# Kernel tuning notes

Hardware: AMD Instinct MI355X
Metric: run time of the kernel (lower is better)

The kernel has to match this reference:

```python
import jax, jax.numpy as jnp
import numpy as np
import math

B, T, D, H = 2, 2048, 1024, 16
DK = D // H
NEG = -1e9  # finite stand-in for -inf causal fill inside the ALiBi bias


def make_alibi_bias(n_heads: int, seq_len: int) -> jnp.ndarray:
    # standard ALiBi slopes: 2^(-8*h/H) for h = 1..H
    slopes = 2.0 ** (-8.0 * (np.arange(1, n_heads + 1) / n_heads))  # [H]
    pos = np.arange(seq_len)
    dist = pos[None, :] - pos[:, None]  # [T,T], j - i
    bias = slopes[:, None, None] * dist[None, :, :]  # [H,T,T], <=0 below diag
    bias = np.where(dist[None] > 0, NEG, bias)  # causal: mask future
    return jnp.asarray(bias, dtype=jnp.float32)


def setup_inputs() -> dict:
    key = jax.random.key(0)
    ks = jax.random.split(key, 8)
    s = 0.02
    return {
        "query": jax.random.normal(ks[0], (B, T, D), jnp.float32),
        "key": jax.random.normal(ks[1], (B, T, D), jnp.float32),
        "value": jax.random.normal(ks[2], (B, T, D), jnp.float32),
        "alibi_bias": make_alibi_bias(H, T),
        "wq": jax.random.normal(ks[3], (D, D), jnp.float32) * s,
        "wk": jax.random.normal(ks[4], (D, D), jnp.float32) * s,
        "wv": jax.random.normal(ks[5], (D, D), jnp.float32) * s,
        "wo": jax.random.normal(ks[6], (D, D), jnp.float32) * s,
        "bo": jnp.zeros((D,), jnp.float32),
    }


def reference(query, key, value, alibi_bias, wq, wk, wv, wo, bo):
    b, tq, d = query.shape
    # linear projections (torch Linear: x @ W^T), split heads -> [B,H,T,d_k]
    def split(x, w):
        y = jnp.einsum('btd,ed->bte', x, w)
        return y.reshape(b, -1, H, DK).transpose(0, 2, 1, 3)
    Q, K, V = split(query, wq), split(key, wk), split(value, wv)
    # scores + ALiBi bias (bias already encodes causality)
    scores = jnp.einsum('bhqd,bhkd->bhqk', Q, K) / math.sqrt(DK)
    scores = scores + alibi_bias[None]  # broadcast over batch
    attn = jax.nn.softmax(scores, axis=-1)
    out = jnp.einsum('bhqk,bhkd->bhqd', attn, V)  # [B,H,Tq,d_k]
    out = out.transpose(0, 2, 1, 3).reshape(b, tq, d)
    return jnp.einsum('btd,ed->bte', out, wo) + bo
```

## Files before the change

kernel.cpp:

```cpp
#include <hip/hip_runtime.h>
#include <hip/hip_bf16.h>
#include <stdint.h>

#define Bc   2
#define Tc   2048
#define Dc   1024
#define Hc   16
#define DKc  64
#define BTc  4096
#define LOG2E 1.44269504088896f

typedef unsigned short u16;
typedef unsigned int u32;
typedef __attribute__((ext_vector_type(8))) short bf16x8;
typedef __attribute__((ext_vector_type(4))) float f32x4;
typedef __attribute__((ext_vector_type(2))) u32 u32x2;

static __device__ __forceinline__ u16 f2bf(float f) {
  union { float f; unsigned u; } v; v.f = f;
  unsigned r = v.u + 0x7fffu + ((v.u >> 16) & 1u);
  return (u16)(r >> 16);
}

static __device__ __forceinline__ u32 cvt_pk_bf16(float lo, float hi) {
  u32 r;
  asm volatile("v_cvt_pk_bf16_f32 %0, %1, %2" : "=v"(r) : "v"(lo), "v"(hi));
  return r;
}

static __device__ __forceinline__ f32x4 mfma16(bf16x8 a, bf16x8 b, f32x4 c) {
  return __builtin_amdgcn_mfma_f32_16x16x32_bf16(a, b, c, 0, 0, 0);
}

__global__ void conv_kernel(const float* __restrict__ q, const float* __restrict__ k,
                            const float* __restrict__ v, const float* __restrict__ wq,
                            const float* __restrict__ wk, const float* __restrict__ wv,
                            const float* __restrict__ wo,
                            u16* __restrict__ Xq, u16* __restrict__ Xk, u16* __restrict__ Xv,
                            u16* __restrict__ Wq, u16* __restrict__ Wk, u16* __restrict__ Wv,
                            u16* __restrict__ Wo) {
  int z = blockIdx.z, bx = blockIdx.x;
  const float* src; u16* dst; int i;
  if (bx < 4096) {
    if (z == 3) return;
    src = z == 0 ? q : z == 1 ? k : v;
    dst = z == 0 ? Xq : z == 1 ? Xk : Xv;
    i = bx * 256 + threadIdx.x;
  } else {
    src = z == 0 ? wq : z == 1 ? wk : z == 2 ? wv : wo;
    dst = z == 0 ? Wq : z == 1 ? Wk : z == 2 ? Wv : Wo;
    i = (bx - 4096) * 256 + threadIdx.x;
  }
  float4 f = ((const float4*)src)[i];
  ushort4 r; r.x = f2bf(f.x); r.y = f2bf(f.y); r.z = f2bf(f.z); r.w = f2bf(f.w);
  ((ushort4*)dst)[i] = r;
}

#define AS1 const __attribute__((address_space(1))) void*
#define AS3 __attribute__((address_space(3))) void*

__global__ __launch_bounds__(256) void gemm_proj(const u16* __restrict__ Xq, const u16* __restrict__ Xk,
                                                 const u16* __restrict__ Xv, const u16* __restrict__ Wq,
                                                 const u16* __restrict__ Wk, const u16* __restrict__ Wv,
                                                 u16* __restrict__ Qh, u16* __restrict__ Kh,
                                                 u16* __restrict__ VTo) {
  __shared__ u16 As[128 * 32];
  __shared__ u16 Bs[128 * 32];
  int z = blockIdx.z;
  const u16* A = z == 0 ? Xq : z == 1 ? Xk : Xv;
  const u16* W = z == 0 ? Wq : z == 1 ? Wk : Wv;
  u16* outp    = z == 0 ? Qh : z == 1 ? Kh : VTo;
  float scale = (z == 0) ? 0.125f * LOG2E : 1.0f;
  int tid = threadIdx.x;
  int lane = tid & 63, wave = tid >> 6;
  int ln = lane & 15, g = lane >> 4;
  int m0 = blockIdx.x * 128, n0 = blockIdx.y * 128;
  int wm = (wave >> 1) * 64, wn = (wave & 1) * 64;
  f32x4 acc[4][4] = {};
  int c0 = tid, c1 = tid + 256;
  const u16* gA0 = A + (size_t)(m0 + (c0 >> 2)) * 1024 + (c0 & 3) * 8;
  const u16* gA1 = A + (size_t)(m0 + (c1 >> 2)) * 1024 + (c1 & 3) * 8;
  const u16* gW0 = W + (size_t)(n0 + (c0 >> 2)) * 1024 + (c0 & 3) * 8;
  const u16* gW1 = W + (size_t)(n0 + (c1 >> 2)) * 1024 + (c1 & 3) * 8;
  for (int k0 = 0; k0 < 1024; k0 += 32) {
    __builtin_amdgcn_global_load_lds((AS1)(gA0 + k0), (AS3)(As + c0 * 8), 16, 0, 0);
    __builtin_amdgcn_global_load_lds((AS1)(gA1 + k0), (AS3)(As + c1 * 8), 16, 0, 0);
    __builtin_amdgcn_global_load_lds((AS1)(gW0 + k0), (AS3)(Bs + c0 * 8), 16, 0, 0);
    __builtin_amdgcn_global_load_lds((AS1)(gW1 + k0), (AS3)(Bs + c1 * 8), 16, 0, 0);
    __syncthreads();
    bf16x8 af[4], bfr[4];
#pragma unroll
    for (int mi = 0; mi < 4; ++mi) af[mi]  = *(const bf16x8*)&As[(wm + mi * 16 + ln) * 32 + g * 8];
#pragma unroll
    for (int ni = 0; ni < 4; ++ni) bfr[ni] = *(const bf16x8*)&Bs[(wn + ni * 16 + ln) * 32 + g * 8];
#pragma unroll
    for (int mi = 0; mi < 4; ++mi)
#pragma unroll
      for (int ni = 0; ni < 4; ++ni)
        acc[mi][ni] = mfma16(af[mi], bfr[ni], acc[mi][ni]);
    __syncthreads();
  }
  if (z == 2) {
#pragma unroll
    for (int mi = 0; mi < 4; ++mi)
#pragma unroll
      for (int ni = 0; ni < 4; ++ni) {
        int t0 = m0 + wm + mi * 16 + g * 4;
        int gn = n0 + wn + ni * 16 + ln;
        size_t bhead = ((size_t)(t0 >> 11)) * Hc + (gn >> 6);
        ushort4 pk;
        pk.x = f2bf(acc[mi][ni][0]); pk.y = f2bf(acc[mi][ni][1]);
        pk.z = f2bf(acc[mi][ni][2]); pk.w = f2bf(acc[mi][ni][3]);
        *(ushort4*)&outp[(bhead * DKc + (gn & 63)) * Tc + (t0 & 2047)] = pk;
      }
  } else {
#pragma unroll
    for (int mi = 0; mi < 4; ++mi)
#pragma unroll
      for (int ni = 0; ni < 4; ++ni)
#pragma unroll
        for (int r = 0; r < 4; ++r) {
          int gm = m0 + wm + mi * 16 + g * 4 + r;
          int gn = n0 + wn + ni * 16 + ln;
          size_t bhead = ((size_t)(gm >> 11)) * Hc + (gn >> 6);
          outp[(bhead * Tc + (gm & 2047)) * DKc + (gn & 63)] = f2bf(acc[mi][ni][r] * scale);
        }
  }
}

__global__ __launch_bounds__(256) void gemm_out(const u16* __restrict__ Ain, const u16* __restrict__ W,
                                                float* __restrict__ of, const float* __restrict__ bias) {
  __shared__ u16 As[64 * 32];
  __shared__ u16 Bs[128 * 32];
  int tid = threadIdx.x;
  int lane = tid & 63, wave = tid >> 6;
  int ln = lane & 15, g = lane >> 4;
  int m0 = blockIdx.x * 64, n0 = blockIdx.y * 128;
  int wm = (wave >> 1) * 32, wn = (wave & 1) * 64;
  f32x4 acc[2][4] = {};
  int ca = tid, cb0 = tid, cb1 = tid + 256;
  const u16* gA  = Ain + (size_t)(m0 + (ca  >> 2)) * 1024 + (ca  & 3) * 8;
  const u16* gW0 = W   + (size_t)(n0 + (cb0 >> 2)) * 1024 + (cb0 & 3) * 8;
  const u16* gW1 = W   + (size_t)(n0 + (cb1 >> 2)) * 1024 + (cb1 & 3) * 8;
  for (int k0 = 0; k0 < 1024; k0 += 32) {
    __builtin_amdgcn_global_load_lds((AS1)(gA  + k0), (AS3)(As + ca  * 8), 16, 0, 0);
    __builtin_amdgcn_global_load_lds((AS1)(gW0 + k0), (AS3)(Bs + cb0 * 8), 16, 0, 0);
    __builtin_amdgcn_global_load_lds((AS1)(gW1 + k0), (AS3)(Bs + cb1 * 8), 16, 0, 0);
    __syncthreads();
    bf16x8 af[2], bfr[4];
#pragma unroll
    for (int mi = 0; mi < 2; ++mi) af[mi]  = *(const bf16x8*)&As[(wm + mi * 16 + ln) * 32 + g * 8];
#pragma unroll
    for (int ni = 0; ni < 4; ++ni) bfr[ni] = *(const bf16x8*)&Bs[(wn + ni * 16 + ln) * 32 + g * 8];
#pragma unroll
    for (int mi = 0; mi < 2; ++mi)
#pragma unroll
      for (int ni = 0; ni < 4; ++ni)
        acc[mi][ni] = mfma16(af[mi], bfr[ni], acc[mi][ni]);
    __syncthreads();
  }
#pragma unroll
  for (int mi = 0; mi < 2; ++mi)
#pragma unroll
    for (int ni = 0; ni < 4; ++ni)
#pragma unroll
      for (int r = 0; r < 4; ++r) {
        int gm = m0 + wm + mi * 16 + g * 4 + r;
        int gn = n0 + wn + ni * 16 + ln;
        of[(size_t)gm * 1024 + gn] = acc[mi][ni][r] + bias[gn];
      }
}

__global__ __launch_bounds__(256, 2) void flash_attn(const u16* __restrict__ Qh,
                                                     const u16* __restrict__ Kh,
                                                     const u16* __restrict__ VT,
                                                     u16* __restrict__ O) {
  __shared__ u16 Ks[2][64 * 64];
  __shared__ u16 Vs[2][64 * 64];
  __shared__ u16 P_lds[8][16][64];
  int pid = blockIdx.x, bh = blockIdx.y;
  int qhi = 16 + pid, qlo = 15 - pid;
  int b = bh >> 4, h = bh & (Hc - 1);
  int tid = threadIdx.x, wave = tid >> 6, lane = tid & 63;
  int ln = lane & 15, g = lane >> 4;
  float slope2 = exp2f(-0.5f * (float)(h + 1)) * LOG2E;

  const u16* gK = Kh + (size_t)bh * Tc * DKc;
  const u16* gV = VT + (size_t)bh * DKc * Tc;
  int c0 = tid, c1 = tid + 256;
  int r0 = c0 >> 3, r1 = c1 >> 3;
  int e0 = ((c0 & 7) << 3) ^ ((r0 & 7) << 3);
  int e1 = ((c1 & 7) << 3) ^ ((r1 & 7) << 3);
  size_t kO0 = (size_t)r0 * DKc + e0, kO1 = (size_t)r1 * DKc + e1;
  size_t vO0 = (size_t)r0 * Tc + e0, vO1 = (size_t)r1 * Tc + e1;

#define STAGE(bufi, ks_) do {                                                                  \
    __builtin_amdgcn_global_load_lds((AS1)(gK + (size_t)(ks_) * DKc + kO0),                    \
                                     (AS3)(&Ks[bufi][c0 * 8]), 16, 0, 0);                      \
    __builtin_amdgcn_global_load_lds((AS1)(gK + (size_t)(ks_) * DKc + kO1),                    \
                                     (AS3)(&Ks[bufi][c1 * 8]), 16, 0, 0);                      \
    __builtin_amdgcn_global_load_lds((AS1)(gV + (size_t)(ks_) + vO0),                          \
                                     (AS3)(&Vs[bufi][c0 * 8]), 16, 0, 0);                      \
    __builtin_amdgcn_global_load_lds((AS1)(gV + (size_t)(ks_) + vO1),                          \
                                     (AS3)(&Vs[bufi][c1 * 8]), 16, 0, 0);                      \
  } while (0)

  int qlocal = wave * 16 + ln;
  int qgH = qhi * 64 + qlocal, qgL = qlo * 64 + qlocal;
  const u16* QpH = Qh + ((size_t)bh * Tc + qgH) * DKc;
  const u16* QpL = Qh + ((size_t)bh * Tc + qgL) * DKc;
  bf16x8 qfH0 = *(const bf16x8*)&QpH[g * 8];
  bf16x8 qfH1 = *(const bf16x8*)&QpH[32 + g * 8];
  bf16x8 qfL0 = *(const bf16x8*)&QpL[g * 8];
  bf16x8 qfL1 = *(const bf16x8*)&QpL[32 + g * 8];

  float vb[4][4];
#pragma unroll
  for (int j = 0; j < 4; ++j)
#pragma unroll
    for (int r = 0; r < 4; ++r)
      vb[j][r] = slope2 * (float)(j * 16 + g * 4 + r);

  f32x4 accH[4] = {}, accL[4] = {};
  float MH = -1e30f, LH = 0.f, ML = -1e30f, LL = 0.f;

  auto tile_step = [&](int buf, int ks, bool diag, bf16x8 qf0, bf16x8 qf1,
                       int qg, float& Mx, float& Lx, f32x4* accO, int pslot) {
    f32x4 s[4] = {};
    __builtin_amdgcn_s_setprio(1);
#pragma unroll
    for (int j = 0; j < 4; ++j) {
      int row = j * 16 + ln, sw = (row & 7) << 3;
      bf16x8 kf0 = *(const bf16x8*)&Ks[buf][row * DKc + ((g * 8) ^ sw)];
      bf16x8 kf1 = *(const bf16x8*)&Ks[buf][row * DKc + ((32 + g * 8) ^ sw)];
      s[j] = mfma16(kf0, qf0, s[j]);
      s[j] = mfma16(kf1, qf1, s[j]);
    }
    __builtin_amdgcn_s_setprio(0);
    float vv[4][4];
    float mloc = -1e30f;
#pragma unroll
    for (int j = 0; j < 4; ++j)
#pragma unroll
      for (int r = 0; r < 4; ++r) {
        float t = s[j][r] + vb[j][r];
        if (diag) t = (j * 16 + g * 4 + r > qlocal) ? -1e30f : t;
        vv[j][r] = t;
        mloc = fmaxf(mloc, t);
      }
    mloc = fmaxf(mloc, __shfl_xor(mloc, 16, 64));
    mloc = fmaxf(mloc, __shfl_xor(mloc, 32, 64));
    float cterm = slope2 * (float)(ks - qg);
    float mc = mloc + cterm;
    if (__any(mc > Mx)) {
      float newM = fmaxf(Mx, mc);
      float sc = __builtin_amdgcn_exp2f(Mx - newM);
      Mx = newM;
      Lx *= sc;
      float scb[4];
#pragma unroll
      for (int r = 0; r < 4; ++r) scb[r] = __shfl(sc, g * 4 + r, 64);
#pragma unroll
      for (int nd = 0; nd < 4; ++nd)
#pragma unroll
        for (int r = 0; r < 4; ++r) accO[nd][r] *= scb[r];
    }
    float dsub = Mx - cterm;
    float rs = 0.f;
#pragma unroll
    for (int j = 0; j < 4; ++j)
#pragma unroll
      for (int r = 0; r < 4; ++r) {
        float p = __builtin_amdgcn_exp2f(vv[j][r] - dsub);
        vv[j][r] = p;
        rs += p;
      }
    Lx += rs;
    char* Prow = (char*)&P_lds[pslot][ln][0];
    int psw = (ln & 7) << 4;
#pragma unroll
    for (int j = 0; j < 4; ++j) {
      u32x2 w;
      w.x = cvt_pk_bf16(vv[j][0], vv[j][1]);
      w.y = cvt_pk_bf16(vv[j][2], vv[j][3]);
      *(u32x2*)(Prow + ((j * 32 + g * 8) ^ psw)) = w;
    }
    __builtin_amdgcn_s_setprio(1);
#pragma unroll
    for (int kk = 0; kk < 2; ++kk) {
      bf16x8 pa = *(const bf16x8*)(Prow + ((kk * 64 + g * 16) ^ psw));
#pragma unroll
      for (int nd = 0; nd < 4; ++nd) {
        int d = nd * 16 + ln, o = kk * 32 + g * 8;
        bf16x8 vf = *(const bf16x8*)&Vs[buf][d * DKc + (o ^ ((d & 7) << 3))];
        accO[nd] = mfma16(pa, vf, accO[nd]);
      }
    }
    __builtin_amdgcn_s_setprio(0);
  };

  STAGE(0, qhi * 64);
  __syncthreads();
  int buf = 0;
  for (int kb = qhi; kb >= 0; --kb) {
    int ks = kb * 64;
    if (kb > 0) STAGE(buf ^ 1, ks - 64);
    tile_step(buf, ks, kb == qhi, qfH0, qfH1, qgH, MH, LH, accH, wave);
    if (kb <= qlo)
      tile_step(buf, ks, kb == qlo, qfL0, qfL1, qgL, ML, LL, accL, wave + 4);
    __syncthreads();
    buf ^= 1;
  }

#pragma unroll
  for (int tile = 0; tile < 2; ++tile) {
    float Lx = tile ? LL : LH;
    f32x4* accO = tile ? accL : accH;
    int qb = tile ? qlo : qhi;
    float Lf = Lx + __shfl_xor(Lx, 16, 64);
    Lf = Lf + __shfl_xor(Lf, 32, 64);
    float linv[4];
#pragma unroll
    for (int r = 0; r < 4; ++r) linv[r] = 1.0f / __shfl(Lf, g * 4 + r, 64);
#pragma unroll
    for (int nd = 0; nd < 4; ++nd)
#pragma unroll
      for (int r = 0; r < 4; ++r) {
        int t = qb * 64 + wave * 16 + g * 4 + r;
        int dcol = h * 64 + nd * 16 + ln;
        O[((size_t)(b * Tc + t)) * Dc + dcol] = f2bf(accO[nd][r] * linv[r]);
      }
  }
#undef STAGE
}

extern "C" void kernel_launch(void* const* d_in, const int* in_sizes, int n_in,
                              void* d_out, int out_size, void* d_ws, size_t ws_size,
                              hipStream_t stream) {
  const float* q  = (const float*)d_in[0];
  const float* k  = (const float*)d_in[1];
  const float* v  = (const float*)d_in[2];
  const float* wq = (const float*)d_in[4];
  const float* wk = (const float*)d_in[5];
  const float* wv = (const float*)d_in[6];
  const float* wo = (const float*)d_in[7];
  const float* bo = (const float*)d_in[8];

  char* ws = (char*)d_ws;
  const size_t MB = 1024 * 1024;
  u16* Xq = (u16*)(ws + 0 * MB);
  u16* Xk = (u16*)(ws + 8 * MB);
  u16* Xv = (u16*)(ws + 16 * MB);
  u16* Wq = (u16*)(ws + 24 * MB);
  u16* Wk = (u16*)(ws + 26 * MB);
  u16* Wv = (u16*)(ws + 28 * MB);
  u16* Wo = (u16*)(ws + 30 * MB);
  u16* Qh = (u16*)(ws + 32 * MB);
  u16* Kh = (u16*)(ws + 40 * MB);
  u16* VT = (u16*)(ws + 48 * MB);
  u16* Ob = (u16*)(ws + 56 * MB);
  float* out = (float*)d_out;

  conv_kernel<<<dim3(4096 + 1024, 1, 4), 256, 0, stream>>>(q, k, v, wq, wk, wv, wo,
                                                           Xq, Xk, Xv, Wq, Wk, Wv, Wo);
  gemm_proj<<<dim3(32, 8, 3), 256, 0, stream>>>(Xq, Xk, Xv, Wq, Wk, Wv, Qh, Kh, VT);
  flash_attn<<<dim3(16, Bc * Hc), 256, 0, stream>>>(Qh, Kh, VT, Ob);
  gemm_out<<<dim3(64, 8), 256, 0, stream>>>(Ob, Wo, out, bo);
}
```

Measured before the change: 127.8 us.

## Fuse fp32-to-bf16 activation conversion into projection GEMM with double buffering

The projection GEMM now reads the fp32 activations directly, converts them to bf16 in registers and writes them to LDS in a k-major layout, so the separate conversion pass over Q/K/V inputs and its intermediate buffers are gone. The GEMM main loop is also double-buffered: register prefetch for A and async global-to-LDS loads for W are issued one stage ahead so they overlap the MFMAs. In exchange the GEMM reads twice as many bytes for A and spends VALU time on conversion inside the loop. Only the weight conversion remains as a standalone kernel.

```diff
diff --git a/kernel.cpp b/kernel.cpp
--- a/kernel.cpp
+++ b/kernel.cpp
@@ -28,29 +28,24 @@
   return r;
 }
 
+static __device__ __forceinline__ u32 cvt_pk_bf16_nv(float lo, float hi) {
+  u32 r;
+  asm("v_cvt_pk_bf16_f32 %0, %1, %2" : "=v"(r) : "v"(lo), "v"(hi));
+  return r;
+}
+
 static __device__ __forceinline__ f32x4 mfma16(bf16x8 a, bf16x8 b, f32x4 c) {
   return __builtin_amdgcn_mfma_f32_16x16x32_bf16(a, b, c, 0, 0, 0);
 }
 
-__global__ void conv_kernel(const float* __restrict__ q, const float* __restrict__ k,
-                            const float* __restrict__ v, const float* __restrict__ wq,
-                            const float* __restrict__ wk, const float* __restrict__ wv,
-                            const float* __restrict__ wo,
-                            u16* __restrict__ Xq, u16* __restrict__ Xk, u16* __restrict__ Xv,
-                            u16* __restrict__ Wq, u16* __restrict__ Wk, u16* __restrict__ Wv,
-                            u16* __restrict__ Wo) {
-  int z = blockIdx.z, bx = blockIdx.x;
-  const float* src; u16* dst; int i;
-  if (bx < 4096) {
-    if (z == 3) return;
-    src = z == 0 ? q : z == 1 ? k : v;
-    dst = z == 0 ? Xq : z == 1 ? Xk : Xv;
-    i = bx * 256 + threadIdx.x;
-  } else {
-    src = z == 0 ? wq : z == 1 ? wk : z == 2 ? wv : wo;
-    dst = z == 0 ? Wq : z == 1 ? Wk : z == 2 ? Wv : Wo;
-    i = (bx - 4096) * 256 + threadIdx.x;
-  }
+__global__ void conv_kernel(const float* __restrict__ wq, const float* __restrict__ wk,
+                            const float* __restrict__ wv, const float* __restrict__ wo,
+                            u16* __restrict__ Wq, u16* __restrict__ Wk,
+                            u16* __restrict__ Wv, u16* __restrict__ Wo) {
+  int z = blockIdx.z;
+  const float* src = z == 0 ? wq : z == 1 ? wk : z == 2 ? wv : wo;
+  u16* dst        = z == 0 ? Wq : z == 1 ? Wk : z == 2 ? Wv : Wo;
+  int i = blockIdx.x * 256 + threadIdx.x;
   float4 f = ((const float4*)src)[i];
   ushort4 r; r.x = f2bf(f.x); r.y = f2bf(f.y); r.z = f2bf(f.z); r.w = f2bf(f.w);
   ((ushort4*)dst)[i] = r;
@@ -59,17 +54,17 @@
 #define AS1 const __attribute__((address_space(1))) void*
 #define AS3 __attribute__((address_space(3))) void*
 
-__global__ __launch_bounds__(256) void gemm_proj(const u16* __restrict__ Xq, const u16* __restrict__ Xk,
-                                                 const u16* __restrict__ Xv, const u16* __restrict__ Wq,
+__global__ __launch_bounds__(256) void gemm_proj(const float* __restrict__ Xq, const float* __restrict__ Xk,
+                                                 const float* __restrict__ Xv, const u16* __restrict__ Wq,
                                                  const u16* __restrict__ Wk, const u16* __restrict__ Wv,
                                                  u16* __restrict__ Qh, u16* __restrict__ Kh,
                                                  u16* __restrict__ VTo) {
-  __shared__ u16 As[128 * 32];
-  __shared__ u16 Bs[128 * 32];
+  __shared__ u16 As[2][128 * 32];
+  __shared__ u16 Bs[2][128 * 32];
   int z = blockIdx.z;
-  const u16* A = z == 0 ? Xq : z == 1 ? Xk : Xv;
-  const u16* W = z == 0 ? Wq : z == 1 ? Wk : Wv;
-  u16* outp    = z == 0 ? Qh : z == 1 ? Kh : VTo;
+  const float* Xf = z == 0 ? Xq : z == 1 ? Xk : Xv;
+  const u16* W    = z == 0 ? Wq : z == 1 ? Wk : Wv;
+  u16* outp       = z == 0 ? Qh : z == 1 ? Kh : VTo;
   float scale = (z == 0) ? 0.125f * LOG2E : 1.0f;
   int tid = threadIdx.x;
   int lane = tid & 63, wave = tid >> 6;
@@ -77,29 +72,66 @@
   int m0 = blockIdx.x * 128, n0 = blockIdx.y * 128;
   int wm = (wave >> 1) * 64, wn = (wave & 1) * 64;
   f32x4 acc[4][4] = {};
+
   int c0 = tid, c1 = tid + 256;
-  const u16* gA0 = A + (size_t)(m0 + (c0 >> 2)) * 1024 + (c0 & 3) * 8;
-  const u16* gA1 = A + (size_t)(m0 + (c1 >> 2)) * 1024 + (c1 & 3) * 8;
   const u16* gW0 = W + (size_t)(n0 + (c0 >> 2)) * 1024 + (c0 & 3) * 8;
   const u16* gW1 = W + (size_t)(n0 + (c1 >> 2)) * 1024 + (c1 & 3) * 8;
-  for (int k0 = 0; k0 < 1024; k0 += 32) {
-    __builtin_amdgcn_global_load_lds((AS1)(gA0 + k0), (AS3)(As + c0 * 8), 16, 0, 0);
-    __builtin_amdgcn_global_load_lds((AS1)(gA1 + k0), (AS3)(As + c1 * 8), 16, 0, 0);
-    __builtin_amdgcn_global_load_lds((AS1)(gW0 + k0), (AS3)(Bs + c0 * 8), 16, 0, 0);
-    __builtin_amdgcn_global_load_lds((AS1)(gW1 + k0), (AS3)(Bs + c1 * 8), 16, 0, 0);
-    __syncthreads();
+  int am = tid & 127, ah = tid >> 7;
+  const float4* gA = (const float4*)(Xf + (size_t)(m0 + am) * 1024 + ah * 16);
+  float4 a4[4];
+
+  auto write_A = [&](int bufi) {
+    uint4 p0, p1;
+    p0.x = cvt_pk_bf16_nv(a4[0].x, a4[0].y);
+    p0.y = cvt_pk_bf16_nv(a4[0].z, a4[0].w);
+    p0.z = cvt_pk_bf16_nv(a4[1].x, a4[1].y);
+    p0.w = cvt_pk_bf16_nv(a4[1].z, a4[1].w);
+    p1.x = cvt_pk_bf16_nv(a4[2].x, a4[2].y);
+    p1.y = cvt_pk_bf16_nv(a4[2].z, a4[2].w);
+    p1.z = cvt_pk_bf16_nv(a4[3].x, a4[3].y);
+    p1.w = cvt_pk_bf16_nv(a4[3].z, a4[3].w);
+    *(uint4*)&As[bufi][((2 * ah) * 128 + am) * 8] = p0;
+    *(uint4*)&As[bufi][((2 * ah + 1) * 128 + am) * 8] = p1;
+  };
+
+#pragma unroll
+  for (int j = 0; j < 4; ++j) a4[j] = gA[j];
+  __builtin_amdgcn_global_load_lds((AS1)(gW0), (AS3)(&Bs[0][c0 * 8]), 16, 0, 0);
+  __builtin_amdgcn_global_load_lds((AS1)(gW1), (AS3)(&Bs[0][c1 * 8]), 16, 0, 0);
+  write_A(0);
+#pragma unroll
+  for (int j = 0; j < 4; ++j) a4[j] = gA[8 + j];
+  __builtin_amdgcn_global_load_lds((AS1)(gW0 + 32), (AS3)(&Bs[1][c0 * 8]), 16, 0, 0);
+  __builtin_amdgcn_global_load_lds((AS1)(gW1 + 32), (AS3)(&Bs[1][c1 * 8]), 16, 0, 0);
+  __syncthreads();
+
+  int cur = 0;
+  for (int it = 0; it < 32; ++it) {
+    if (it < 31) write_A(cur ^ 1);
+    if (it < 30) {
+#pragma unroll
+      for (int j = 0; j < 4; ++j) a4[j] = gA[(it + 2) * 8 + j];
+    }
     bf16x8 af[4], bfr[4];
 #pragma unroll
-    for (int mi = 0; mi < 4; ++mi) af[mi]  = *(const bf16x8*)&As[(wm + mi * 16 + ln) * 32 + g * 8];
-#pragma unroll
-    for (int ni = 0; ni < 4; ++ni) bfr[ni] = *(const bf16x8*)&Bs[(wn + ni * 16 + ln) * 32 + g * 8];
+    for (int mi = 0; mi < 4; ++mi)
+      af[mi] = *(const bf16x8*)&As[cur][(g * 128 + wm + mi * 16 + ln) * 8];
+#pragma unroll
+    for (int ni = 0; ni < 4; ++ni)
+      bfr[ni] = *(const bf16x8*)&Bs[cur][(wn + ni * 16 + ln) * 32 + g * 8];
 #pragma unroll
     for (int mi = 0; mi < 4; ++mi)
 #pragma unroll
       for (int ni = 0; ni < 4; ++ni)
         acc[mi][ni] = mfma16(af[mi], bfr[ni], acc[mi][ni]);
     __syncthreads();
-  }
+    if (it < 30) {
+      __builtin_amdgcn_global_load_lds((AS1)(gW0 + (it + 2) * 32), (AS3)(&Bs[cur][c0 * 8]), 16, 0, 0);
+      __builtin_amdgcn_global_load_lds((AS1)(gW1 + (it + 2) * 32), (AS3)(&Bs[cur][c1 * 8]), 16, 0, 0);
+    }
+    cur ^= 1;
+  }
+
   if (z == 2) {
 #pragma unroll
     for (int mi = 0; mi < 4; ++mi)
@@ -348,9 +380,6 @@
 
   char* ws = (char*)d_ws;
   const size_t MB = 1024 * 1024;
-  u16* Xq = (u16*)(ws + 0 * MB);
-  u16* Xk = (u16*)(ws + 8 * MB);
-  u16* Xv = (u16*)(ws + 16 * MB);
   u16* Wq = (u16*)(ws + 24 * MB);
   u16* Wk = (u16*)(ws + 26 * MB);
   u16* Wv = (u16*)(ws + 28 * MB);
@@ -361,9 +390,8 @@
   u16* Ob = (u16*)(ws + 56 * MB);
   float* out = (float*)d_out;
 
-  conv_kernel<<<dim3(4096 + 1024, 1, 4), 256, 0, stream>>>(q, k, v, wq, wk, wv, wo,
-                                                           Xq, Xk, Xv, Wq, Wk, Wv, Wo);
-  gemm_proj<<<dim3(32, 8, 3), 256, 0, stream>>>(Xq, Xk, Xv, Wq, Wk, Wv, Qh, Kh, VT);
+  conv_kernel<<<dim3(1024, 1, 4), 256, 0, stream>>>(wq, wk, wv, wo, Wq, Wk, Wv, Wo);
+  gemm_proj<<<dim3(32, 8, 3), 256, 0, stream>>>(q, k, v, Wq, Wk, Wv, Qh, Kh, VT);
   flash_attn<<<dim3(16, Bc * Hc), 256, 0, stream>>>(Qh, Kh, VT, Ob);
   gemm_out<<<dim3(64, 8), 256, 0, stream>>>(Ob, Wo, out, bo);
 }
```

Result: slower. 132.1 us (+3.4%).
